# Performance work log

Measured on AMD Instinct MI355X. Metric: run time of the kernel, lower is better.

## Reference

```python
import jax, jax.numpy as jnp
import numpy as np

HEAD_NUM = 4
B, S, D = 8, 1024, 512


def setup_inputs() -> dict:
    k = jax.random.key(0)
    kq, kk, kv = jax.random.split(k, 3)
    return {
        "query": jax.random.normal(kq, (B, S, D), dtype=jnp.float32),
        "key": jax.random.normal(kk, (B, S, D), dtype=jnp.float32),
        "value": jax.random.normal(kv, (B, S, D), dtype=jnp.float32),
    }


def _corr_attention(q, k, v):
    # q,k,v: [B, H, S, hd]
    score = jnp.einsum('bhqd,bhkd->bhqk', q, k)  # raw dot products
    len_q = jnp.sqrt(jnp.sum(q * q, axis=-1))    # [B,H,S]
    len_k = jnp.sqrt(jnp.sum(k * k, axis=-1))    # [B,H,S]
    score = score / (len_q[..., :, None] * len_k[..., None, :])  # cosine similarity
    signal = jnp.sign(score)
    flat = jnp.abs(score).reshape(-1)            # global flatten across B,H,S,S
    n = flat.shape[0]
    idx = jnp.argsort(-flat)                     # descending sort indices
    prob = (jnp.arange(n, dtype=flat.dtype) + 1.0) / n  # (1/n, 2/n, ..., 1)
    ranked = flat.at[idx].set(prob)              # rank-transform: largest -> smallest prob
    score = (-jnp.log(ranked)).reshape(signal.shape) * signal
    return jnp.einsum('bhqk,bhkd->bhqd', score, v)


def reference(query, key, value):
    b, s, d = query.shape
    h = HEAD_NUM
    q = query.reshape(b, s, h, -1).transpose(0, 2, 1, 3)
    k = key.reshape(b, s, h, -1).transpose(0, 2, 1, 3)
    v = value.reshape(b, s, h, -1).transpose(0, 2, 1, 3)
    out = _corr_attention(q, k, v)               # [B,H,S,hd]
    return out.transpose(0, 2, 1, 3).reshape(b, s, d)
```

## Files before the change

### kernel.cpp

```cpp
#include <hip/hip_runtime.h>
#include <math.h>

#define BB 8
#define SS 1024
#define DD 512
#define HH 4
#define HD 128
#define N_SC (BB*HH*SS*SS)

#define NB 8192
#define BINS 13107.2f
#define NBLK 2048
#define NP2 32

#define OFF_QN    0
#define SZ_QN     ((size_t)BB*SS*DD*2)
#define OFF_KN    (OFF_QN + SZ_QN)
#define OFF_VT    (OFF_KN + SZ_QN)
#define OFF_PARTS (OFF_VT + SZ_QN)
#define SZ_PARTS  ((size_t)NBLK*(NB/4)*4)
#define OFF_WMAG  (OFF_PARTS + SZ_PARTS)
#define OFF_PART2 (OFF_WMAG + (size_t)NB*2)

typedef __bf16 bf16x8 __attribute__((ext_vector_type(8)));
typedef float  f32x4  __attribute__((ext_vector_type(4)));
typedef unsigned short ushort_t;

__device__ __forceinline__ unsigned bf16rne(float x) {
  unsigned b = __float_as_uint(x);
  return (b + 0x7FFFu + ((b >> 16) & 1u)) >> 16;
}
__device__ __forceinline__ unsigned sbin(float s) {
  return (unsigned)fminf(fabsf(s)*BINS, 8191.0f);
}

__global__ __launch_bounds__(256) void prep_vt_kernel(
    const float* __restrict__ q, const float* __restrict__ k,
    const float* __restrict__ v,
    unsigned* __restrict__ qn, unsigned* __restrict__ kn,
    unsigned* __restrict__ vt) {
  __shared__ float T[64][65];
  int t = threadIdx.x;
  if (blockIdx.x < 16384) {
    int lane = t & 63;
    int row = blockIdx.x*4 + (t >> 6);
    const float* src; unsigned* dst; int r;
    if (row < 32768) { src = q; dst = qn; r = row; }
    else             { src = k; dst = kn; r = row - 32768; }
    int b = r >> 12, s = (r >> 2) & 1023, h = r & 3;
    float2 vv = *(const float2*)(src + ((size_t)(b*1024 + s))*512 + h*128 + lane*2);
    float sum = vv.x*vv.x + vv.y*vv.y;
    #pragma unroll
    for (int off = 32; off; off >>= 1) sum += __shfl_xor(sum, off, 64);
    float inv = rsqrtf(sum);
    unsigned u = bf16rne(vv.x*inv) | (bf16rne(vv.y*inv) << 16);
    dst[(size_t)((b*4 + h)*1024 + s)*64 + lane] = u;
  } else {
    int vb = blockIdx.x - 16384;
    int s0 = (vb & 15)*64, d0 = ((vb >> 4) & 1)*64, bh = vb >> 5;
    int b = bh >> 2, h = bh & 3;
    #pragma unroll
    for (int i = 0; i < 16; i++) {
      int idx = t + i*256, rs = idx >> 6, cd = idx & 63;
      T[rs][cd] = v[((size_t)(b*1024 + s0 + rs))*512 + h*128 + d0 + cd];
    }
    __syncthreads();
    #pragma unroll
    for (int i = 0; i < 8; i++) {
      int idx = t + i*256, rd = idx >> 5, c2 = (idx & 31)*2;
      unsigned u = bf16rne(T[c2][rd]) | (bf16rne(T[c2+1][rd]) << 16);
      vt[(size_t)(bh*128 + d0 + rd)*512 + (s0 + c2)/2] = u;
    }
  }
}

__global__ __launch_bounds__(256) void scores_hist_kernel(
    const ushort_t* __restrict__ qn, const ushort_t* __restrict__ kn,
    unsigned* __restrict__ parts) {
  __shared__ ushort_t Qs[128*128];
  __shared__ ushort_t Ks[128*128];
  __shared__ unsigned h8[NB/4];
  int t = threadIdx.x;
  int L = blockIdx.x;
  int bh = L & 31, tile = L >> 5;
  int sq0 = (tile >> 3)*128, sk0 = (tile & 7)*128;

  #pragma unroll
  for (int i = 0; i < 8; i++) h8[t + i*256] = 0;

  const uint4* qg = (const uint4*)qn + (size_t)(bh*1024 + sq0)*16;
  const uint4* kg = (const uint4*)kn + (size_t)(bh*1024 + sk0)*16;
  #pragma unroll
  for (int i = 0; i < 8; i++) {
    int idx = t + i*256, row = idx >> 4, g = idx & 15;
    int sw = g ^ (row & 15);
    *(uint4*)&Qs[row*128 + sw*8] = qg[row*16 + g];
    *(uint4*)&Ks[row*128 + sw*8] = kg[row*16 + g];
  }
  __syncthreads();

  int w = t >> 6, lane = t & 63, m16 = lane & 15, q2 = lane >> 4;
  int wm = (w >> 1)*64, wn = (w & 1)*64;
  f32x4 acc[4][4];
  #pragma unroll
  for (int i = 0; i < 4; i++)
    #pragma unroll
    for (int j = 0; j < 4; j++) acc[i][j] = (f32x4){0.f,0.f,0.f,0.f};

  #pragma unroll
  for (int ks = 0; ks < 4; ks++) {
    int sw = ((ks*4 + q2) ^ m16)*8;
    bf16x8 a[4], bb[4];
    #pragma unroll
    for (int i = 0; i < 4; i++) a[i]  = *(const bf16x8*)&Qs[(wm + i*16 + m16)*128 + sw];
    #pragma unroll
    for (int j = 0; j < 4; j++) bb[j] = *(const bf16x8*)&Ks[(wn + j*16 + m16)*128 + sw];
    #pragma unroll
    for (int i = 0; i < 4; i++)
      #pragma unroll
      for (int j = 0; j < 4; j++)
        acc[i][j] = __builtin_amdgcn_mfma_f32_16x16x32_bf16(a[i], bb[j], acc[i][j], 0, 0, 0);
  }

  #pragma unroll
  for (int i = 0; i < 4; i++)
    #pragma unroll
    for (int j = 0; j < 4; j++)
      #pragma unroll
      for (int p = 0; p < 4; p++) {
        unsigned bin = sbin(acc[i][j][p]);
        atomicAdd(&h8[bin >> 2], 1u << ((bin & 3)*8));
      }
  __syncthreads();

  unsigned* dst = parts + (size_t)L*(NB/4);
  #pragma unroll
  for (int i = 0; i < 8; i++) dst[t + i*256] = h8[t + i*256];
}

__global__ __launch_bounds__(256) void reduce1_kernel(
    const unsigned* __restrict__ parts, unsigned* __restrict__ parts2) {
  int g = blockIdx.x*256 + threadIdx.x;
  int p0 = blockIdx.y*64;
  unsigned s0 = 0, s1 = 0, s2 = 0, s3 = 0;
  #pragma unroll 8
  for (int p = p0; p < p0 + 64; p++) {
    unsigned w = parts[(size_t)p*(NB/4) + g];
    s0 += w & 0xFFu; s1 += (w >> 8) & 0xFFu;
    s2 += (w >> 16) & 0xFFu; s3 += w >> 24;
  }
  uint4 o = {s0, s1, s2, s3};
  ((uint4*)parts2)[(size_t)blockIdx.y*(NB/4) + g] = o;
}

__global__ __launch_bounds__(1024) void scan_kernel(
    const unsigned* __restrict__ parts2, ushort_t* __restrict__ wmag) {
  __shared__ unsigned d[1024];
  int t = threadIdx.x;
  unsigned loc[8] = {0,0,0,0,0,0,0,0};
  #pragma unroll 4
  for (int p = 0; p < NP2; p++) {
    uint4 a = ((const uint4*)parts2)[(size_t)p*(NB/4) + t*2];
    uint4 b2 = ((const uint4*)parts2)[(size_t)p*(NB/4) + t*2 + 1];
    loc[0] += a.x;  loc[1] += a.y;  loc[2] += a.z;  loc[3] += a.w;
    loc[4] += b2.x; loc[5] += b2.y; loc[6] += b2.z; loc[7] += b2.w;
  }
  unsigned tot = 0;
  #pragma unroll
  for (int j = 0; j < 8; j++) tot += loc[j];
  d[t] = tot; __syncthreads();
  for (int off = 1; off < 1024; off <<= 1) {
    unsigned x = (t >= off) ? d[t - off] : 0u;
    __syncthreads();
    d[t] += x;
    __syncthreads();
  }
  unsigned run = d[t] - tot;
  const float inv_n = 1.0f / (float)N_SC;
  #pragma unroll
  for (int j = 0; j < 8; j++) {
    run += loc[j];
    float rm = (float)(N_SC - run) + 0.5f*(float)(loc[j] + 1u);
    wmag[t*8 + j] = (ushort_t)bf16rne(-logf(rm * inv_n));
  }
}

__global__ __launch_bounds__(256) void out_kernel(
    const ushort_t* __restrict__ qn, const ushort_t* __restrict__ kn,
    const ushort_t* __restrict__ wmag, const ushort_t* __restrict__ vt,
    float* __restrict__ out) {
  __shared__ ushort_t Qs[64*128];
  __shared__ ushort_t Ks[128*128];
  __shared__ ushort_t Ws[64*128];
  __shared__ ushort_t Wl[NB];
  int t = threadIdx.x;
  int L = blockIdx.x;
  int bh = L & 31, q0 = (L >> 5)*64;
  int b = bh >> 2, h = bh & 3;

  #pragma unroll
  for (int i = 0; i < 4; i++)
    ((uint4*)Wl)[t + i*256] = ((const uint4*)wmag)[t + i*256];

  const uint4* qg = (const uint4*)qn + (size_t)(bh*1024 + q0)*16;
  #pragma unroll
  for (int i = 0; i < 4; i++) {
    int idx = t + i*256, row = idx >> 4, g = idx & 15;
    *(uint4*)&Qs[row*128 + (g ^ (row & 15))*8] = qg[row*16 + g];
  }

  int w = t >> 6, lane = t & 63, m16 = lane & 15, q2 = lane >> 4;
  int wq = (w >> 1)*32, wd = (w & 1)*64;
  f32x4 oacc[2][4];
  #pragma unroll
  for (int i = 0; i < 2; i++)
    #pragma unroll
    for (int j = 0; j < 4; j++) oacc[i][j] = (f32x4){0.f,0.f,0.f,0.f};

  for (int kc = 0; kc < 8; kc++) {
    const uint4* kg = (const uint4*)kn + (size_t)(bh*1024 + kc*128)*16;
    #pragma unroll
    for (int i = 0; i < 8; i++) {
      int idx = t + i*256, row = idx >> 4, g = idx & 15;
      *(uint4*)&Ks[row*128 + (g ^ (row & 15))*8] = kg[row*16 + g];
    }
    __syncthreads();

    f32x4 sacc[2][4];
    #pragma unroll
    for (int i = 0; i < 2; i++)
      #pragma unroll
      for (int j = 0; j < 4; j++) sacc[i][j] = (f32x4){0.f,0.f,0.f,0.f};
    #pragma unroll
    for (int ks = 0; ks < 4; ks++) {
      int sw = ((ks*4 + q2) ^ m16)*8;
      bf16x8 a[2], bb[4];
      #pragma unroll
      for (int i = 0; i < 2; i++) a[i]  = *(const bf16x8*)&Qs[(wq + i*16 + m16)*128 + sw];
      #pragma unroll
      for (int j = 0; j < 4; j++) bb[j] = *(const bf16x8*)&Ks[(wd + j*16 + m16)*128 + sw];
      #pragma unroll
      for (int i = 0; i < 2; i++)
        #pragma unroll
        for (int j = 0; j < 4; j++)
          sacc[i][j] = __builtin_amdgcn_mfma_f32_16x16x32_bf16(a[i], bb[j], sacc[i][j], 0, 0, 0);
    }
    __syncthreads();

    #pragma unroll
    for (int i = 0; i < 2; i++)
      #pragma unroll
      for (int j = 0; j < 4; j++)
        #pragma unroll
        for (int p = 0; p < 4; p++) {
          float s = sacc[i][j][p];
          unsigned wm = (s == 0.f) ? 0u
                        : (unsigned)Wl[sbin(s)] | ((s < 0.f) ? 0x8000u : 0u);
          int row = wq + i*16 + q2*4 + p;
          int col = wd + j*16 + m16;
          Ws[row*128 + ((col >> 3) ^ (row & 15))*8 + (col & 7)] = (ushort_t)wm;
        }
    __syncthreads();

    const uint4* vg = (const uint4*)vt;
    #pragma unroll
    for (int ks = 0; ks < 4; ks++) {
      int sw = ((ks*4 + q2) ^ m16)*8;
      bf16x8 a[2], bb[4];
      #pragma unroll
      for (int i = 0; i < 2; i++) a[i] = *(const bf16x8*)&Ws[(wq + i*16 + m16)*128 + sw];
      #pragma unroll
      for (int j = 0; j < 4; j++)
        bb[j] = *(const bf16x8*)&vg[(size_t)(bh*128 + wd + j*16 + m16)*128 + kc*16 + ks*4 + q2];
      #pragma unroll
      for (int i = 0; i < 2; i++)
        #pragma unroll
        for (int j = 0; j < 4; j++)
          oacc[i][j] = __builtin_amdgcn_mfma_f32_16x16x32_bf16(a[i], bb[j], oacc[i][j], 0, 0, 0);
    }
  }

  #pragma unroll
  for (int i = 0; i < 2; i++)
    #pragma unroll
    for (int p = 0; p < 4; p++) {
      int qrow = q0 + wq + i*16 + q2*4 + p;
      #pragma unroll
      for (int j = 0; j < 4; j++) {
        int dcol = wd + j*16 + m16;
        out[(size_t)(b*1024 + qrow)*512 + h*128 + dcol] = oacc[i][j][p];
      }
    }
}

extern "C" void kernel_launch(void* const* d_in, const int* in_sizes, int n_in,
                              void* d_out, int out_size, void* d_ws, size_t ws_size,
                              hipStream_t stream) {
  const float* q = (const float*)d_in[0];
  const float* k = (const float*)d_in[1];
  const float* v = (const float*)d_in[2];
  float* out = (float*)d_out;
  char* ws = (char*)d_ws;

  unsigned* qn    = (unsigned*)(ws + OFF_QN);
  unsigned* kn    = (unsigned*)(ws + OFF_KN);
  unsigned* vtb   = (unsigned*)(ws + OFF_VT);
  unsigned* parts = (unsigned*)(ws + OFF_PARTS);
  ushort_t* wmag  = (ushort_t*)(ws + OFF_WMAG);
  unsigned* part2 = (unsigned*)(ws + OFF_PART2);

  hipLaunchKernelGGL(prep_vt_kernel, dim3(17408), dim3(256), 0, stream, q, k, v, qn, kn, vtb);
  hipLaunchKernelGGL(scores_hist_kernel, dim3(NBLK), dim3(256), 0, stream,
                     (const ushort_t*)qn, (const ushort_t*)kn, parts);
  hipLaunchKernelGGL(reduce1_kernel, dim3(8, NP2), dim3(256), 0, stream, parts, part2);
  hipLaunchKernelGGL(scan_kernel, dim3(1), dim3(1024), 0, stream, part2, wmag);
  hipLaunchKernelGGL(out_kernel, dim3(512), dim3(256), 0, stream,
                     (const ushort_t*)qn, (const ushort_t*)kn, wmag,
                     (const ushort_t*)vtb, out);
}
```

Measured before the change: 192.2 us.

## Materialize bf16 score matrix once instead of recomputing QK^T in output pass

The scores kernel now writes the full bf16 cosine-score matrix (64 MB) to workspace alongside building the histogram. The output kernel reads these stored scores, maps them through the rank lookup table, and runs only the score×V MFMA, dropping the second QK^T GEMM and its Q/K shared-memory staging. V is now staged in shared memory per key chunk. This trades recomputation for a large extra global write and read, and rounds scores to bf16 before binning, which can shift bin assignments slightly.

```diff
diff --git a/kernel.cpp b/kernel.cpp
--- a/kernel.cpp
+++ b/kernel.cpp
@@ -13,7 +13,9 @@
 #define NBLK 2048
 #define NP2 32
 
-#define OFF_QN    0
+#define OFF_S     0
+#define SZ_S      ((size_t)N_SC*2)
+#define OFF_QN    (OFF_S + SZ_S)
 #define SZ_QN     ((size_t)BB*SS*DD*2)
 #define OFF_KN    (OFF_QN + SZ_QN)
 #define OFF_VT    (OFF_KN + SZ_QN)
@@ -76,7 +78,7 @@
 
 __global__ __launch_bounds__(256) void scores_hist_kernel(
     const ushort_t* __restrict__ qn, const ushort_t* __restrict__ kn,
-    unsigned* __restrict__ parts) {
+    ushort_t* __restrict__ S, unsigned* __restrict__ parts) {
   __shared__ ushort_t Qs[128*128];
   __shared__ ushort_t Ks[128*128];
   __shared__ unsigned h8[NB/4];
@@ -122,15 +124,21 @@
         acc[i][j] = __builtin_amdgcn_mfma_f32_16x16x32_bf16(a[i], bb[j], acc[i][j], 0, 0, 0);
   }
 
+  size_t Sbase = (size_t)bh << 20;
   #pragma unroll
   for (int i = 0; i < 4; i++)
     #pragma unroll
-    for (int j = 0; j < 4; j++)
-      #pragma unroll
-      for (int p = 0; p < 4; p++) {
-        unsigned bin = sbin(acc[i][j][p]);
+    for (int p = 0; p < 4; p++) {
+      int row = sq0 + wm + i*16 + q2*4 + p;
+      #pragma unroll
+      for (int j = 0; j < 4; j++) {
+        int col = sk0 + wn + j*16 + m16;
+        unsigned u = bf16rne(acc[i][j][p]);
+        S[Sbase + ((size_t)row << 10) + col] = (ushort_t)u;
+        unsigned bin = sbin(__uint_as_float(u << 16));
         atomicAdd(&h8[bin >> 2], 1u << ((bin & 3)*8));
       }
+    }
   __syncthreads();
 
   unsigned* dst = parts + (size_t)L*(NB/4);
@@ -186,12 +194,9 @@
 }
 
 __global__ __launch_bounds__(256) void out_kernel(
-    const ushort_t* __restrict__ qn, const ushort_t* __restrict__ kn,
-    const ushort_t* __restrict__ wmag, const ushort_t* __restrict__ vt,
-    float* __restrict__ out) {
-  __shared__ ushort_t Qs[64*128];
-  __shared__ ushort_t Ks[128*128];
-  __shared__ ushort_t Ws[64*128];
+    const ushort_t* __restrict__ S, const ushort_t* __restrict__ wmag,
+    const ushort_t* __restrict__ vt, float* __restrict__ out) {
+  __shared__ ushort_t Vs[128*128];
   __shared__ ushort_t Wl[NB];
   int t = threadIdx.x;
   int L = blockIdx.x;
@@ -202,95 +207,55 @@
   for (int i = 0; i < 4; i++)
     ((uint4*)Wl)[t + i*256] = ((const uint4*)wmag)[t + i*256];
 
-  const uint4* qg = (const uint4*)qn + (size_t)(bh*1024 + q0)*16;
-  #pragma unroll
-  for (int i = 0; i < 4; i++) {
-    int idx = t + i*256, row = idx >> 4, g = idx & 15;
-    *(uint4*)&Qs[row*128 + (g ^ (row & 15))*8] = qg[row*16 + g];
-  }
-
   int w = t >> 6, lane = t & 63, m16 = lane & 15, q2 = lane >> 4;
-  int wq = (w >> 1)*32, wd = (w & 1)*64;
-  f32x4 oacc[2][4];
-  #pragma unroll
-  for (int i = 0; i < 2; i++)
-    #pragma unroll
-    for (int j = 0; j < 4; j++) oacc[i][j] = (f32x4){0.f,0.f,0.f,0.f};
+  int qw = q0 + w*16;
+  const ushort_t* Srow = S + ((size_t)(bh*1024 + qw + m16) << 10);
+  const uint4* vg = (const uint4*)vt + (size_t)bh*128*128;
+
+  f32x4 oacc[8];
+  #pragma unroll
+  for (int j = 0; j < 8; j++) oacc[j] = (f32x4){0.f,0.f,0.f,0.f};
 
   for (int kc = 0; kc < 8; kc++) {
-    const uint4* kg = (const uint4*)kn + (size_t)(bh*1024 + kc*128)*16;
     #pragma unroll
     for (int i = 0; i < 8; i++) {
       int idx = t + i*256, row = idx >> 4, g = idx & 15;
-      *(uint4*)&Ks[row*128 + (g ^ (row & 15))*8] = kg[row*16 + g];
-    }
-    __syncthreads();
-
-    f32x4 sacc[2][4];
-    #pragma unroll
-    for (int i = 0; i < 2; i++)
-      #pragma unroll
-      for (int j = 0; j < 4; j++) sacc[i][j] = (f32x4){0.f,0.f,0.f,0.f};
+      *(uint4*)&Vs[row*128 + (g ^ (row & 15))*8] = vg[row*128 + kc*16 + g];
+    }
+    __syncthreads();
+
     #pragma unroll
     for (int ks = 0; ks < 4; ks++) {
+      uint4 sv = *(const uint4*)&Srow[kc*128 + ks*32 + q2*8];
+      unsigned sc[4] = {sv.x, sv.y, sv.z, sv.w};
+      union { bf16x8 v; unsigned u[4]; } af;
+      #pragma unroll
+      for (int m = 0; m < 4; m++) {
+        float flo = __uint_as_float(sc[m] << 16);
+        float fhi = __uint_as_float(sc[m] & 0xFFFF0000u);
+        unsigned wlo = (flo == 0.f) ? 0u
+                       : (unsigned)Wl[sbin(flo)] | ((flo < 0.f) ? 0x8000u : 0u);
+        unsigned whi = (fhi == 0.f) ? 0u
+                       : (unsigned)Wl[sbin(fhi)] | ((fhi < 0.f) ? 0x8000u : 0u);
+        af.u[m] = wlo | (whi << 16);
+      }
       int sw = ((ks*4 + q2) ^ m16)*8;
-      bf16x8 a[2], bb[4];
-      #pragma unroll
-      for (int i = 0; i < 2; i++) a[i]  = *(const bf16x8*)&Qs[(wq + i*16 + m16)*128 + sw];
-      #pragma unroll
-      for (int j = 0; j < 4; j++) bb[j] = *(const bf16x8*)&Ks[(wd + j*16 + m16)*128 + sw];
-      #pragma unroll
-      for (int i = 0; i < 2; i++)
-        #pragma unroll
-        for (int j = 0; j < 4; j++)
-          sacc[i][j] = __builtin_amdgcn_mfma_f32_16x16x32_bf16(a[i], bb[j], sacc[i][j], 0, 0, 0);
-    }
-    __syncthreads();
-
-    #pragma unroll
-    for (int i = 0; i < 2; i++)
-      #pragma unroll
-      for (int j = 0; j < 4; j++)
-        #pragma unroll
-        for (int p = 0; p < 4; p++) {
-          float s = sacc[i][j][p];
-          unsigned wm = (s == 0.f) ? 0u
-                        : (unsigned)Wl[sbin(s)] | ((s < 0.f) ? 0x8000u : 0u);
-          int row = wq + i*16 + q2*4 + p;
-          int col = wd + j*16 + m16;
-          Ws[row*128 + ((col >> 3) ^ (row & 15))*8 + (col & 7)] = (ushort_t)wm;
-        }
-    __syncthreads();
-
-    const uint4* vg = (const uint4*)vt;
-    #pragma unroll
-    for (int ks = 0; ks < 4; ks++) {
-      int sw = ((ks*4 + q2) ^ m16)*8;
-      bf16x8 a[2], bb[4];
-      #pragma unroll
-      for (int i = 0; i < 2; i++) a[i] = *(const bf16x8*)&Ws[(wq + i*16 + m16)*128 + sw];
-      #pragma unroll
-      for (int j = 0; j < 4; j++)
-        bb[j] = *(const bf16x8*)&vg[(size_t)(bh*128 + wd + j*16 + m16)*128 + kc*16 + ks*4 + q2];
-      #pragma unroll
-      for (int i = 0; i < 2; i++)
-        #pragma unroll
-        for (int j = 0; j < 4; j++)
-          oacc[i][j] = __builtin_amdgcn_mfma_f32_16x16x32_bf16(a[i], bb[j], oacc[i][j], 0, 0, 0);
-    }
-  }
-
-  #pragma unroll
-  for (int i = 0; i < 2; i++)
-    #pragma unroll
-    for (int p = 0; p < 4; p++) {
-      int qrow = q0 + wq + i*16 + q2*4 + p;
-      #pragma unroll
-      for (int j = 0; j < 4; j++) {
-        int dcol = wd + j*16 + m16;
-        out[(size_t)(b*1024 + qrow)*512 + h*128 + dcol] = oacc[i][j][p];
+      #pragma unroll
+      for (int j = 0; j < 8; j++) {
+        bf16x8 bb = *(const bf16x8*)&Vs[(j*16 + m16)*128 + sw];
+        oacc[j] = __builtin_amdgcn_mfma_f32_16x16x32_bf16(af.v, bb, oacc[j], 0, 0, 0);
       }
     }
+    __syncthreads();
+  }
+
+  #pragma unroll
+  for (int p = 0; p < 4; p++) {
+    int qrow = qw + q2*4 + p;
+    #pragma unroll
+    for (int j = 0; j < 8; j++)
+      out[(size_t)(b*1024 + qrow)*512 + h*128 + j*16 + m16] = oacc[j][p];
+  }
 }
 
 extern "C" void kernel_launch(void* const* d_in, const int* in_sizes, int n_in,
@@ -302,6 +267,7 @@
   float* out = (float*)d_out;
   char* ws = (char*)d_ws;
 
+  ushort_t* Sbuf  = (ushort_t*)(ws + OFF_S);
   unsigned* qn    = (unsigned*)(ws + OFF_QN);
   unsigned* kn    = (unsigned*)(ws + OFF_KN);
   unsigned* vtb   = (unsigned*)(ws + OFF_VT);
@@ -311,10 +277,9 @@
 
   hipLaunchKernelGGL(prep_vt_kernel, dim3(17408), dim3(256), 0, stream, q, k, v, qn, kn, vtb);
   hipLaunchKernelGGL(scores_hist_kernel, dim3(NBLK), dim3(256), 0, stream,
-                     (const ushort_t*)qn, (const ushort_t*)kn, parts);
+                     (const ushort_t*)qn, (const ushort_t*)kn, Sbuf, parts);
   hipLaunchKernelGGL(reduce1_kernel, dim3(8, NP2), dim3(256), 0, stream, parts, part2);
   hipLaunchKernelGGL(scan_kernel, dim3(1), dim3(1024), 0, stream, part2, wmag);
   hipLaunchKernelGGL(out_kernel, dim3(512), dim3(256), 0, stream,
-                     (const ushort_t*)qn, (const ushort_t*)kn, wmag,
-                     (const ushort_t*)vtb, out);
-}
+                     (const ushort_t*)Sbuf, wmag, (const ushort_t*)vtb, out);
+}
```

Measured after the change: 176.6 us. 1.09x faster.
